# Kernel optimization log

Measured on AMD Instinct MI355X. Metric: run time of the kernel, lower is better.

The kernel has to match this reference:

```python
import jax, jax.numpy as jnp
import numpy as np

BS, M, D, D_EM, K_RET = 32, 32768, 1024, 128, 32
EPS = 1e-12

def unit_normalize(x):
    return x / jnp.sqrt(jnp.sum(x * x, axis=-1, keepdims=True) + EPS)

def setup_inputs() -> dict:
    key = jax.random.key(0)
    ks = jax.random.split(key, 12)
    s = lambda fan_in: 1.0 / np.sqrt(fan_in)
    return {
        "x": jax.random.normal(ks[0], (BS, D), jnp.float32),
        "y_wm": jax.random.normal(ks[1], (BS, D), jnp.float32),
        "em_K": unit_normalize(jax.random.normal(ks[2], (BS, M, D_EM), jnp.float32)),
        "em_V": jax.random.normal(ks[3], (BS, M, D_EM), jnp.float32) * 0.01,
        "em_S": jax.random.uniform(ks[4], (BS, M), jnp.float32),  # all > 0 (active)
        "Wq_em_w": jax.random.normal(ks[5], (2 * D, D_EM), jnp.float32) * s(2 * D),
        "Wq_em_b": jnp.zeros((D_EM,), jnp.float32),
        "Wq_cross_w": jax.random.normal(ks[6], (D, D_EM), jnp.float32) * s(D),
        "Wq_cross_b": jnp.zeros((D_EM,), jnp.float32),
        "Wo_w": jax.random.normal(ks[7], (D_EM, D), jnp.float32) * s(D_EM),
        "Wo_b": jnp.zeros((D,), jnp.float32),
        "ln_g": jnp.ones((D_EM,), jnp.float32),
        "ln_b": jnp.zeros((D_EM,), jnp.float32),
        "ffn1_w": jax.random.normal(ks[8], (D_EM, 4 * D_EM), jnp.float32) * s(D_EM),
        "ffn1_b": jnp.zeros((4 * D_EM,), jnp.float32),
        "ffn2_w": jax.random.normal(ks[9], (4 * D_EM, D_EM), jnp.float32) * s(4 * D_EM),
        "ffn2_b": jnp.zeros((D_EM,), jnp.float32),
    }

def layernorm(x, g, b):
    mu = jnp.mean(x, axis=-1, keepdims=True)
    var = jnp.mean((x - mu) ** 2, axis=-1, keepdims=True)
    return (x - mu) * jax.lax.rsqrt(var + 1e-5) * g + b

def reference(x, y_wm, em_K, em_V, em_S, Wq_em_w, Wq_em_b, Wq_cross_w, Wq_cross_b,
              Wo_w, Wo_b, ln_g, ln_b, ffn1_w, ffn1_b, ffn2_w, ffn2_b):
    # query over concatenated (x, y_wm), unit-normalized
    q = unit_normalize(jnp.concatenate([x, y_wm], axis=-1) @ Wq_em_w + Wq_em_b)  # [BS, D_em]
    # masked cosine similarity scan over all M slots
    scores = jnp.einsum('bd,bmd->bm', q, em_K)                                   # [BS, M]
    scores = jnp.where(em_S > 0, scores, -jnp.inf)
    topk_scores, topk_idx = jax.lax.top_k(scores, K_RET)                         # [BS, k]
    V_top = jnp.take_along_axis(em_V, topk_idx[:, :, None], axis=1)              # [BS, k, D_em]
    # cross-attention read over retrieved slots
    q_cross = x @ Wq_cross_w + Wq_cross_b                                        # [BS, D_em]
    attn = jnp.einsum('bd,bkd->bk', q_cross, V_top) * (D_EM ** -0.5) + topk_scores
    attn = jnp.where(jnp.isneginf(topk_scores), -jnp.inf, attn)
    attn = jnp.nan_to_num(jax.nn.softmax(attn, axis=-1), nan=0.0)
    out = jnp.einsum('bk,bkd->bd', attn, V_top)                                  # [BS, D_em]
    # readout FFN (residual), exact GELU as in torch default
    h = layernorm(out, ln_g, ln_b)
    out = out + (jax.nn.gelu(h @ ffn1_w + ffn1_b, approximate=False) @ ffn2_w + ffn2_b)
    return out @ Wo_w + Wo_b                                                     # [BS, D]
```

## Files before the change

kernel.cpp:

```cpp
#include <hip/hip_runtime.h>
#include <math.h>

constexpr int kM  = 32768;
constexpr int kD  = 1024;
constexpr int kDE = 128;
constexpr int kK  = 32;
constexpr int kCap = 2048;
constexpr int kLBuf = 128;
constexpr float kT0 = 0.20f;

typedef float f4 __attribute__((ext_vector_type(4)));

__device__ __forceinline__ int score_bin(float s) {
  float w = (s + 1.0f) * 128.0f;
  w = fminf(fmaxf(w, 0.0f), 255.0f);
  return (int)w;
}
__device__ __forceinline__ unsigned long long pack_key(float s, int idx) {
  unsigned u = __float_as_uint(s);
  u = (u & 0x80000000u) ? ~u : (u | 0x80000000u);
  return ((unsigned long long)u << 32) | (unsigned)(~idx);
}

__global__ __launch_bounds__(1024) void qproj_kernel(
    const float* __restrict__ x, const float* __restrict__ y,
    const float* __restrict__ Wqe, const float* __restrict__ bqe,
    const float* __restrict__ Wqc, const float* __restrict__ bqc,
    float* __restrict__ q, float* __restrict__ qc,
    unsigned int* __restrict__ gcnt, unsigned int* __restrict__ gflag) {
  const int b = blockIdx.x, t = threadIdx.x;
  const int s = t >> 7, j = t & 127;

  if (t == 0) { gcnt[b] = 0u; gflag[b] = 0u; }

  const float* xb = x + b * kD;
  const float* yb = y + b * kD;

  const float* src1 = (s < 4) ? xb : yb;
  const int off1 = (s < 4) ? s * 256 : s * 256 - 1024;
  const int wb1 = s * 256;
  float a1[4] = {0.f, 0.f, 0.f, 0.f};
#pragma unroll 8
  for (int i0 = 0; i0 < 256; i0 += 4) {
#pragma unroll
    for (int u = 0; u < 4; ++u)
      a1[u] += src1[off1 + i0 + u] * Wqe[(wb1 + i0 + u) * kDE + j];
  }
  const int r2 = s * 128;
  float a2[4] = {0.f, 0.f, 0.f, 0.f};
#pragma unroll 8
  for (int i0 = 0; i0 < 128; i0 += 4) {
#pragma unroll
    for (int u = 0; u < 4; ++u)
      a2[u] += xb[r2 + i0 + u] * Wqc[(r2 + i0 + u) * kDE + j];
  }

  __shared__ float p1[8][128];
  __shared__ float p2[8][128];
  __shared__ float redn[2];
  p1[s][j] = (a1[0] + a1[1]) + (a1[2] + a1[3]);
  p2[s][j] = (a2[0] + a2[1]) + (a2[2] + a2[3]);
  __syncthreads();

  float a = 0.f, c = 0.f;
  if (t < 128) {
    a = bqe[t];
    c = bqc[t];
#pragma unroll
    for (int ss = 0; ss < 8; ++ss) { a += p1[ss][t]; c += p2[ss][t]; }
  }
  float sq = a * a;
#pragma unroll
  for (int m = 1; m < 64; m <<= 1) sq += __shfl_xor(sq, m);
  if (t == 0 || t == 64) redn[t >> 6] = sq;
  __syncthreads();
  if (t < 128) {
    const float inv = 1.f / sqrtf(redn[0] + redn[1] + 1e-12f);
    q[b * kDE + t] = a * inv;
    qc[b * kDE + t] = c;
  }
}

__global__ __launch_bounds__(256) void scores_kernel(
    const float* __restrict__ emK, const float* __restrict__ emS,
    const float* __restrict__ q, float* __restrict__ sc,
    unsigned int* __restrict__ gcnt, unsigned long long* __restrict__ gcand,
    unsigned int* __restrict__ gflag) {
  const int b = blockIdx.y, chunk = blockIdx.x;
  const int wave = threadIdx.x >> 6;
  const int lane = threadIdx.x & 63;
  const int half = lane >> 5;
  const int l32 = lane & 31;

  __shared__ unsigned int lcnt;
  __shared__ unsigned int lbase;
  __shared__ unsigned long long lbuf[kLBuf];
  if (threadIdx.x == 0) lcnt = 0u;
  __syncthreads();

  const float4 qf = *reinterpret_cast<const float4*>(q + b * kDE + l32 * 4);
  const int rowbase = chunk * 512 + wave * 128;
  const float* Kb = emK + (size_t)b * kM * kDE;
  const float* Sb = emS + (size_t)b * kM;
  float* scb = sc + (size_t)b * kM;

  for (int it = 0; it < 8; ++it) {
    const int A = rowbase + it * 16 + half * 8;
    const float* p = Kb + (size_t)A * kDE + l32 * 4;
    const f4 k0 = __builtin_nontemporal_load((const f4*)(p));
    const f4 k1 = __builtin_nontemporal_load((const f4*)(p + kDE));
    const f4 k2 = __builtin_nontemporal_load((const f4*)(p + 2 * kDE));
    const f4 k3 = __builtin_nontemporal_load((const f4*)(p + 3 * kDE));
    const f4 k4 = __builtin_nontemporal_load((const f4*)(p + 4 * kDE));
    const f4 k5 = __builtin_nontemporal_load((const f4*)(p + 5 * kDE));
    const f4 k6 = __builtin_nontemporal_load((const f4*)(p + 6 * kDE));
    const f4 k7 = __builtin_nontemporal_load((const f4*)(p + 7 * kDE));

    float d0 = fmaf(k0.w, qf.w, fmaf(k0.z, qf.z, fmaf(k0.y, qf.y, k0.x * qf.x)));
    float d1 = fmaf(k1.w, qf.w, fmaf(k1.z, qf.z, fmaf(k1.y, qf.y, k1.x * qf.x)));
    float d2 = fmaf(k2.w, qf.w, fmaf(k2.z, qf.z, fmaf(k2.y, qf.y, k2.x * qf.x)));
    float d3 = fmaf(k3.w, qf.w, fmaf(k3.z, qf.z, fmaf(k3.y, qf.y, k3.x * qf.x)));
    float d4 = fmaf(k4.w, qf.w, fmaf(k4.z, qf.z, fmaf(k4.y, qf.y, k4.x * qf.x)));
    float d5 = fmaf(k5.w, qf.w, fmaf(k5.z, qf.z, fmaf(k5.y, qf.y, k5.x * qf.x)));
    float d6 = fmaf(k6.w, qf.w, fmaf(k6.z, qf.z, fmaf(k6.y, qf.y, k6.x * qf.x)));
    float d7 = fmaf(k7.w, qf.w, fmaf(k7.z, qf.z, fmaf(k7.y, qf.y, k7.x * qf.x)));

    d0 += __shfl_xor(d0, 16); d1 += __shfl_xor(d1, 16);
    d2 += __shfl_xor(d2, 16); d3 += __shfl_xor(d3, 16);
    d4 += __shfl_xor(d4, 16); d5 += __shfl_xor(d5, 16);
    d6 += __shfl_xor(d6, 16); d7 += __shfl_xor(d7, 16);
    float w0 = (l32 & 16) ? d4 : d0;
    float w1 = (l32 & 16) ? d5 : d1;
    float w2 = (l32 & 16) ? d6 : d2;
    float w3 = (l32 & 16) ? d7 : d3;
    w0 += __shfl_xor(w0, 8); w1 += __shfl_xor(w1, 8);
    w2 += __shfl_xor(w2, 8); w3 += __shfl_xor(w3, 8);
    float u0 = (l32 & 8) ? w2 : w0;
    float u1 = (l32 & 8) ? w3 : w1;
    u0 += __shfl_xor(u0, 4); u1 += __shfl_xor(u1, 4);
    float z = (l32 & 4) ? u1 : u0;
    z += __shfl_xor(z, 2);
    z += __shfl_xor(z, 1);

    const float sv = Sb[A + (l32 >> 2)];
    if ((l32 & 3) == 0) {
      const int row = A + (l32 >> 2);
      const float val = (sv > 0.f) ? z : -INFINITY;
      __builtin_nontemporal_store(val, &scb[row]);
      if (val >= kT0) {
        const unsigned pos = atomicAdd(&lcnt, 1u);
        if (pos < (unsigned)kLBuf) lbuf[pos] = pack_key(val, row);
      }
    }
  }
  __syncthreads();

  const unsigned c = min(lcnt, (unsigned)kLBuf);
  if (threadIdx.x == 0) {
    lbase = atomicAdd(&gcnt[b], c);
    if (lcnt > (unsigned)kLBuf) atomicOr(&gflag[b], 1u);
  }
  __syncthreads();
  const unsigned base = lbase;
  for (unsigned i = threadIdx.x; i < c; i += 256) {
    const unsigned pos = base + i;
    if (pos < (unsigned)kCap) gcand[(size_t)b * kCap + pos] = lbuf[i];
  }
}

__global__ __launch_bounds__(512) void finish_kernel(
    const float* __restrict__ sc, const unsigned int* __restrict__ gcnt,
    const unsigned long long* __restrict__ gcand,
    const unsigned int* __restrict__ gflag,
    const float* __restrict__ emV, const float* __restrict__ qc,
    const float* __restrict__ lng, const float* __restrict__ lnb,
    const float* __restrict__ f1w, const float* __restrict__ f1b,
    const float* __restrict__ f2w, const float* __restrict__ f2b,
    const float* __restrict__ Wo, const float* __restrict__ Wob,
    float* __restrict__ out) {
  const int b = blockIdx.x, t = threadIdx.x;
  const int wave = t >> 6, lane = t & 63;

  __shared__ unsigned long long ck[kCap];
  __shared__ int nS;
  __shared__ float outvS[32];
  __shared__ int outiS[32];
  __shared__ float Vt[32][128];
  __shared__ float qcl[128];
  __shared__ float wgt[32];
  __shared__ float hS[128];
  __shared__ float y1S[512];
  __shared__ float p2S[4][128];
  __shared__ float o2S[128];
  __shared__ float redA[2];
  __shared__ float redB[2];

  const unsigned cnt = gcnt[b];
  const unsigned flag = gflag[b];
  const float* scb = sc + (size_t)b * kM;
  if (t < 128) qcl[t] = qc[b * kDE + t];
  if (t < 32) { outvS[t] = -INFINITY; outiS[t] = 0; }

  if (flag == 0u && cnt >= 32u && cnt <= (unsigned)kCap) {
    for (unsigned i = t; i < cnt; i += 512)
      ck[i] = gcand[(size_t)b * kCap + i];
    if (t == 0) nS = (int)cnt;
  } else {
    __shared__ unsigned int shist[256];
    __shared__ int Bsh;
    __shared__ unsigned int cnt2;
    if (t < 256) shist[t] = 0u;
    if (t == 0) { Bsh = 0; cnt2 = 0u; }
    __syncthreads();
    for (int i = t; i < kM; i += 512)
      atomicAdd(&shist[score_bin(scb[i])], 1u);
    __syncthreads();
    for (int off = 1; off < 256; off <<= 1) {
      unsigned v = 0;
      if (t < 256) {
        v = shist[t];
        if (t + off < 256) v += shist[t + off];
      }
      __syncthreads();
      if (t < 256) shist[t] = v;
      __syncthreads();
    }
    if (t < 256 && shist[t] >= 32u) atomicMax(&Bsh, t);
    __syncthreads();
    const int B = Bsh;
    for (int i = t; i < kM; i += 512) {
      const float s = scb[i];
      if (score_bin(s) >= B) {
        const unsigned pos = atomicAdd(&cnt2, 1u);
        if (pos < (unsigned)kCap) ck[pos] = pack_key(s, i);
      }
    }
    __syncthreads();
    if (t == 0) nS = (int)min(cnt2, (unsigned)kCap);
  }
  __syncthreads();
  const int n = nS;

  unsigned long long mykey0 = 0, mykey1 = 0, mykey2 = 0, mykey3 = 0;
  if (t < n) mykey0 = ck[t];
  if (t + 512 < n) mykey1 = ck[t + 512];
  if (t + 1024 < n) mykey2 = ck[t + 1024];
  if (t + 1536 < n) mykey3 = ck[t + 1536];
  int r0 = 0, r1 = 0, r2 = 0, r3 = 0;
  for (int i = 0; i < n; ++i) {
    const unsigned long long o = ck[i];
    r0 += (o > mykey0);
    r1 += (o > mykey1);
    r2 += (o > mykey2);
    r3 += (o > mykey3);
  }
  auto emit = [&](unsigned long long key, int rank, int slot) {
    if (slot < n && rank < 32) {
      const unsigned mono = (unsigned)(key >> 32);
      const unsigned u = (mono & 0x80000000u) ? (mono & 0x7fffffffu) : ~mono;
      outvS[rank] = __uint_as_float(u);
      outiS[rank] = (int)(~(unsigned)key);
    }
  };
  emit(mykey0, r0, t);
  emit(mykey1, r1, t + 512);
  emit(mykey2, r2, t + 1024);
  emit(mykey3, r3, t + 1536);
  __syncthreads();

  const float* Vb = emV + (size_t)b * kM * kDE;
#pragma unroll
  for (int e = t; e < 32 * 128; e += 512) {
    const int r = e >> 7, ccol = e & 127;
    Vt[r][ccol] = Vb[(size_t)outiS[r] * kDE + ccol];
  }
  __syncthreads();

#pragma unroll
  for (int kk2 = 0; kk2 < 4; ++kk2) {
    const int k = wave * 4 + kk2;
    float p = Vt[k][2 * lane] * qcl[2 * lane] + Vt[k][2 * lane + 1] * qcl[2 * lane + 1];
#pragma unroll
    for (int m = 1; m < 64; m <<= 1) p += __shfl_xor(p, m);
    if (lane == 0) {
      const float tv = outvS[k];
      wgt[k] = (tv == -INFINITY) ? -INFINITY : fmaf(p, 0.08838834764831845f, tv);
    }
  }
  __syncthreads();

  if (t < 32) {
    const float lg = wgt[t];
    float mx = lg;
#pragma unroll
    for (int m = 1; m < 32; m <<= 1) mx = fmaxf(mx, __shfl_xor(mx, m));
    float e = (mx == -INFINITY || lg == -INFINITY) ? 0.f : __expf(lg - mx);
    float ssum = e;
#pragma unroll
    for (int m = 1; m < 32; m <<= 1) ssum += __shfl_xor(ssum, m);
    wgt[t] = (ssum > 0.f) ? e / ssum : 0.f;
  }
  __syncthreads();

  float od = 0.f;
  if (t < 128) {
#pragma unroll 8
    for (int k = 0; k < 32; ++k) od += wgt[k] * Vt[k][t];
  }
  float s1 = (t < 128) ? od : 0.f;
  float s2 = (t < 128) ? od * od : 0.f;
#pragma unroll
  for (int m = 1; m < 64; m <<= 1) {
    s1 += __shfl_xor(s1, m);
    s2 += __shfl_xor(s2, m);
  }
  if (lane == 0 && wave < 2) { redA[wave] = s1; redB[wave] = s2; }
  __syncthreads();
  const float sum1 = redA[0] + redA[1];
  const float sum2 = redB[0] + redB[1];
  const float mu = sum1 * (1.f / 128.f);
  const float var = sum2 * (1.f / 128.f) - mu * mu;
  const float rstd = 1.f / sqrtf(var + 1e-5f);
  if (t < 128) hS[t] = (od - mu) * rstd * lng[t] + lnb[t];
  __syncthreads();

  {
    float acc = f1b[t];
#pragma unroll 8
    for (int d = 0; d < 128; ++d) acc += hS[d] * f1w[(size_t)d * 512 + t];
    y1S[t] = 0.5f * acc * (1.f + erff(acc * 0.7071067811865476f));
  }
  __syncthreads();

  {
    const int g = t >> 7, ccol = t & 127;
    float acc = 0.f;
#pragma unroll 8
    for (int jj = 0; jj < 128; ++jj)
      acc += y1S[g * 128 + jj] * f2w[(size_t)(g * 128 + jj) * 128 + ccol];
    p2S[g][ccol] = acc;
  }
  __syncthreads();
  if (t < 128)
    o2S[t] = od + f2b[t] + ((p2S[0][t] + p2S[1][t]) + (p2S[2][t] + p2S[3][t]));
  __syncthreads();

  float acc0 = Wob[t], acc1 = Wob[t + 512];
#pragma unroll 8
  for (int d = 0; d < 128; ++d) {
    const float hv = o2S[d];
    acc0 += hv * Wo[(size_t)d * kD + t];
    acc1 += hv * Wo[(size_t)d * kD + t + 512];
  }
  out[(size_t)b * kD + t] = acc0;
  out[(size_t)b * kD + t + 512] = acc1;
}

extern "C" void kernel_launch(void* const* d_in, const int* in_sizes, int n_in,
                              void* d_out, int out_size, void* d_ws, size_t ws_size,
                              hipStream_t stream) {
  const float* x   = (const float*)d_in[0];
  const float* y   = (const float*)d_in[1];
  const float* emK = (const float*)d_in[2];
  const float* emV = (const float*)d_in[3];
  const float* emS = (const float*)d_in[4];
  const float* Wqe = (const float*)d_in[5];
  const float* bqe = (const float*)d_in[6];
  const float* Wqc = (const float*)d_in[7];
  const float* bqc = (const float*)d_in[8];
  const float* Wo  = (const float*)d_in[9];
  const float* Wob = (const float*)d_in[10];
  const float* lng = (const float*)d_in[11];
  const float* lnb = (const float*)d_in[12];
  const float* f1w = (const float*)d_in[13];
  const float* f1b = (const float*)d_in[14];
  const float* f2w = (const float*)d_in[15];
  const float* f2b = (const float*)d_in[16];
  float* out = (float*)d_out;

  float* ws = (float*)d_ws;
  float* q  = ws;
  float* qc = ws + 4096;
  float* sc = ws + 8192;
  unsigned int* gcnt  = (unsigned int*)(ws + 8192 + 32 * kM);
  unsigned int* gflag = gcnt + 32;
  unsigned long long* gcand =
      (unsigned long long*)(gcnt + 64);

  hipLaunchKernelGGL(qproj_kernel, dim3(32), dim3(1024), 0, stream,
                     x, y, Wqe, bqe, Wqc, bqc, q, qc, gcnt, gflag);
  hipLaunchKernelGGL(scores_kernel, dim3(64, 32), dim3(256), 0, stream,
                     emK, emS, q, sc, gcnt, gcand, gflag);
  hipLaunchKernelGGL(finish_kernel, dim3(32), dim3(512), 0, stream,
                     sc, gcnt, gcand, gflag, emV, qc, lng, lnb,
                     f1w, f1b, f2w, f2b, Wo, Wob, out);
}
```

Measured before the change: 157.6 us.

## Split query projection across 256 blocks with last-block atomic reduction

The query projection moves from 32 blocks of 1024 threads to 256 blocks of 256 threads. Each block computes a slice of partial dot products, writes them to workspace, and the last block to finish for each batch row (found through an atomic counter) reduces the partials and normalizes. This spreads the weight-streaming work over more compute units. The cost is a memset launch to clear the counters, global partial-sum traffic, and an atomic handoff between blocks.

```diff
diff --git a/kernel.cpp b/kernel.cpp
--- a/kernel.cpp
+++ b/kernel.cpp
@@ -22,53 +22,62 @@
   return ((unsigned long long)u << 32) | (unsigned)(~idx);
 }
 
-__global__ __launch_bounds__(1024) void qproj_kernel(
+__global__ __launch_bounds__(256) void qproj_fused(
     const float* __restrict__ x, const float* __restrict__ y,
     const float* __restrict__ Wqe, const float* __restrict__ bqe,
     const float* __restrict__ Wqc, const float* __restrict__ bqc,
+    float* __restrict__ pq, float* __restrict__ pqc,
     float* __restrict__ q, float* __restrict__ qc,
-    unsigned int* __restrict__ gcnt, unsigned int* __restrict__ gflag) {
-  const int b = blockIdx.x, t = threadIdx.x;
-  const int s = t >> 7, j = t & 127;
-
-  if (t == 0) { gcnt[b] = 0u; gflag[b] = 0u; }
-
-  const float* xb = x + b * kD;
-  const float* yb = y + b * kD;
-
-  const float* src1 = (s < 4) ? xb : yb;
-  const int off1 = (s < 4) ? s * 256 : s * 256 - 1024;
-  const int wb1 = s * 256;
-  float a1[4] = {0.f, 0.f, 0.f, 0.f};
-#pragma unroll 8
-  for (int i0 = 0; i0 < 256; i0 += 4) {
-#pragma unroll
-    for (int u = 0; u < 4; ++u)
-      a1[u] += src1[off1 + i0 + u] * Wqe[(wb1 + i0 + u) * kDE + j];
-  }
-  const int r2 = s * 128;
-  float a2[4] = {0.f, 0.f, 0.f, 0.f};
-#pragma unroll 8
-  for (int i0 = 0; i0 < 128; i0 += 4) {
-#pragma unroll
-    for (int u = 0; u < 4; ++u)
-      a2[u] += xb[r2 + i0 + u] * Wqc[(r2 + i0 + u) * kDE + j];
-  }
-
-  __shared__ float p1[8][128];
-  __shared__ float p2[8][128];
-  __shared__ float redn[2];
-  p1[s][j] = (a1[0] + a1[1]) + (a1[2] + a1[3]);
-  p2[s][j] = (a2[0] + a2[1]) + (a2[2] + a2[3]);
-  __syncthreads();
+    unsigned* __restrict__ gdone) {
+  const int blk = blockIdx.x, t = threadIdx.x;
+  const int qb = blk >> 3, slice = blk & 7;
+  const int h = t >> 7, j = t & 127;
+  const int S = slice * 2 + h;
+
+  const float* srcA = (S < 8) ? (x + qb * kD + S * 128)
+                              : (y + qb * kD + (S - 8) * 128);
+  const float* wA = Wqe + (size_t)(S * 128) * kDE + j;
+  float s0 = 0.f, s1 = 0.f, s2 = 0.f, s3 = 0.f;
+#pragma unroll 8
+  for (int i = 0; i < 128; i += 4) {
+    s0 += srcA[i]     * wA[(size_t)(i)     * kDE];
+    s1 += srcA[i + 1] * wA[(size_t)(i + 1) * kDE];
+    s2 += srcA[i + 2] * wA[(size_t)(i + 2) * kDE];
+    s3 += srcA[i + 3] * wA[(size_t)(i + 3) * kDE];
+  }
+  pq[(qb * 16 + S) * 128 + j] = (s0 + s1) + (s2 + s3);
+
+  const float* srcB = x + qb * kD + S * 64;
+  const float* wB = Wqc + (size_t)(S * 64) * kDE + j;
+  float c0 = 0.f, c1 = 0.f, c2 = 0.f, c3 = 0.f;
+#pragma unroll 8
+  for (int i = 0; i < 64; i += 4) {
+    c0 += srcB[i]     * wB[(size_t)(i)     * kDE];
+    c1 += srcB[i + 1] * wB[(size_t)(i + 1) * kDE];
+    c2 += srcB[i + 2] * wB[(size_t)(i + 2) * kDE];
+    c3 += srcB[i + 3] * wB[(size_t)(i + 3) * kDE];
+  }
+  pqc[(qb * 16 + S) * 128 + j] = (c0 + c1) + (c2 + c3);
+
+  __syncthreads();
+  __shared__ unsigned doneS;
+  if (t == 0)
+    doneS = __hip_atomic_fetch_add(&gdone[qb], 1u, __ATOMIC_ACQ_REL,
+                                   __HIP_MEMORY_SCOPE_AGENT);
+  __syncthreads();
+  if (doneS != 7u) return;
 
   float a = 0.f, c = 0.f;
   if (t < 128) {
     a = bqe[t];
     c = bqc[t];
 #pragma unroll
-    for (int ss = 0; ss < 8; ++ss) { a += p1[ss][t]; c += p2[ss][t]; }
-  }
+    for (int S2 = 0; S2 < 16; ++S2) {
+      a += pq[(qb * 16 + S2) * 128 + t];
+      c += pqc[(qb * 16 + S2) * 128 + t];
+    }
+  }
+  __shared__ float redn[2];
   float sq = a * a;
 #pragma unroll
   for (int m = 1; m < 64; m <<= 1) sq += __shfl_xor(sq, m);
@@ -76,8 +85,8 @@
   __syncthreads();
   if (t < 128) {
     const float inv = 1.f / sqrtf(redn[0] + redn[1] + 1e-12f);
-    q[b * kDE + t] = a * inv;
-    qc[b * kDE + t] = c;
+    q[qb * kDE + t] = a * inv;
+    qc[qb * kDE + t] = c;
   }
 }
 
@@ -379,16 +388,21 @@
   float* out = (float*)d_out;
 
   float* ws = (float*)d_ws;
-  float* q  = ws;
-  float* qc = ws + 4096;
-  float* sc = ws + 8192;
-  unsigned int* gcnt  = (unsigned int*)(ws + 8192 + 32 * kM);
-  unsigned int* gflag = gcnt + 32;
+  float* pq  = ws;
+  float* pqc = ws + 65536;
+  float* q   = ws + 131072;
+  float* qc  = ws + 135168;
+  float* sc  = ws + 139264;
+  unsigned* meta = (unsigned*)(ws + 1187840);
+  unsigned* gcnt  = meta;
+  unsigned* gflag = meta + 32;
+  unsigned* gdone = meta + 64;
   unsigned long long* gcand =
-      (unsigned long long*)(gcnt + 64);
-
-  hipLaunchKernelGGL(qproj_kernel, dim3(32), dim3(1024), 0, stream,
-                     x, y, Wqe, bqe, Wqc, bqc, q, qc, gcnt, gflag);
+      (unsigned long long*)(ws + 1187968);
+
+  hipMemsetAsync(meta, 0, 96 * sizeof(unsigned), stream);
+  hipLaunchKernelGGL(qproj_fused, dim3(256), dim3(256), 0, stream,
+                     x, y, Wqe, bqe, Wqc, bqc, pq, pqc, q, qc, gdone);
   hipLaunchKernelGGL(scores_kernel, dim3(64, 32), dim3(256), 0, stream,
                      emK, emS, q, sc, gcnt, gcand, gflag);
   hipLaunchKernelGGL(finish_kernel, dim3(32), dim3(512), 0, stream,
```

After: 149.1 us. 5.4% less time.
